# Performance work log

Hardware: AMD Instinct MI355X
Metric: run time of the kernel (lower is better)

## Reference

```python
import jax, jax.numpy as jnp
import numpy as np

DIM = 128
N_VAR = 100000
N_CON = 100000
N_NODES = 200000
N_EDGES = 640000


def setup_inputs() -> dict:
    key = jax.random.key(0)
    ks = jax.random.split(key, 25)
    d = DIM
    u = lambda k, s: jax.random.uniform(k, s, jnp.float32, -0.1, 0.1)
    inp = {
        "var_node_features": jax.random.normal(ks[0], (N_VAR, 2), jnp.float32),
        "con_node_features": jax.random.normal(ks[1], (N_CON, 2), jnp.float32),
        "node_types": jax.random.randint(ks[2], (N_NODES,), 0, 2),
        "assoc_var": jnp.arange(N_VAR),
        "assoc_con": N_VAR + jnp.arange(N_CON),
        "edge_index": jax.random.randint(ks[3], (2, N_EDGES), 0, N_NODES),
        "edge_types": jax.random.randint(ks[4], (N_EDGES,), 0, 2),
        "edge_features": jax.random.normal(ks[5], (N_EDGES, 1), jnp.float32),
        "var_w1": u(ks[6], (2, d)), "var_b1": u(ks[7], (d,)),
        "var_w2": u(ks[8], (d, d)), "var_b2": u(ks[9], (d,)),
        "con_w1": u(ks[10], (2, d)), "con_b1": u(ks[11], (d,)),
        "con_w2": u(ks[12], (d, d)), "con_b2": u(ks[13], (d,)),
    }
    for i, k0 in zip((1, 2, 3), (14, 17, 20)):
        inp[f"basis{i}"] = u(ks[k0], (1, d, d))      # num_bases=1
        inp[f"att{i}"] = u(ks[k0 + 1], (2, 1))       # num_relations=2
        inp[f"root{i}"] = u(ks[k0 + 2], (d, d))
        inp[f"bias{i}"] = jnp.zeros((d,), jnp.float32)
    inp["fc1_w"] = u(ks[23], (4 * d, d))
    inp["fc1_b"] = jnp.zeros((d,), jnp.float32)
    inp["fc4_w"] = u(ks[24], (d, 1))
    inp["fc4_b"] = jnp.zeros((1,), jnp.float32)
    return inp


def rgcn(x, src, dst, etype, basis, att, root, bias):
    # basis: [1, d, d], att: [2, 1] -> per-relation weights [2, d, d]
    d = x.shape[-1]
    w = (att @ basis.reshape(basis.shape[0], -1)).reshape(2, d, d)
    xj = x[src]  # [E, d] gather
    # only 2 relations: two GEMMs + select (avoids [E,d,d] materialization)
    msg = jnp.where((etype == 0)[:, None], xj @ w[0], xj @ w[1])
    s = jax.ops.segment_sum(msg, dst, num_segments=N_NODES)
    cnt = jax.ops.segment_sum(jnp.ones((dst.shape[0],), x.dtype), dst, num_segments=N_NODES)
    agg = s / jnp.maximum(cnt, 1.0)[:, None]  # mean aggregation
    return agg + x @ root + bias


def reference(var_node_features, con_node_features, node_types, assoc_var, assoc_con,
              edge_index, edge_types, edge_features,
              var_w1, var_b1, var_w2, var_b2,
              con_w1, con_b1, con_w2, con_b2,
              basis1, att1, root1, bias1,
              basis2, att2, root2, bias2,
              basis3, att3, root3, bias3,
              fc1_w, fc1_b, fc4_w, fc4_b):
    n = jnp.maximum(var_node_features @ var_w1 + var_b1, 0.0) @ var_w2 + var_b2
    e = jnp.maximum(con_node_features @ con_w1 + con_b1, 0.0) @ con_w2 + con_b2
    x = jnp.zeros((node_types.shape[0], n.shape[-1]), n.dtype)
    x = x.at[assoc_var].set(n).at[assoc_con].set(e)
    src, dst = edge_index[0], edge_index[1]
    x1 = jax.nn.relu(rgcn(x, src, dst, edge_types, basis1, att1, root1, bias1))
    x2 = jax.nn.relu(rgcn(x1, src, dst, edge_types, basis2, att2, root2, bias2))
    x3 = jax.nn.relu(rgcn(x2, src, dst, edge_types, basis3, att3, root3, bias3))
    h = jnp.concatenate([x, x1, x2, x3], axis=-1)[assoc_var]  # [n_var, 4d]
    h = jax.nn.relu(h @ fc1_w + fc1_b)
    # dropout p=0.5 is identity in eval mode
    return (h @ fc4_w + fc4_b)[:, 0]
```

## Files before the change

kernel.cpp:

```cpp
#include <hip/hip_runtime.h>
#include <hip/hip_bf16.h>

#define D 128
#define NV 100000
#define NC 100000
#define NN 200000
#define NE 640000

typedef __attribute__((ext_vector_type(4))) float f32x4;
typedef __attribute__((ext_vector_type(8))) short bf16x8;

static __device__ __forceinline__ unsigned short f2b(float f) {
    __hip_bfloat16 h = __float2bfloat16(f);
    union { __hip_bfloat16 h; unsigned short u; } c; c.h = h; return c.u;
}
static __device__ __forceinline__ float b2f(unsigned short b) {
    union { unsigned int u; float f; } c; c.u = ((unsigned int)b) << 16; return c.f;
}

template<bool RELU>
static __device__ __forceinline__ void split8v(const float f[8], bf16x8& ah, bf16x8& al)
{
    union { unsigned short s[8]; bf16x8 v; } ph, pl;
    #pragma unroll
    for (int j = 0; j < 8; ++j) {
        float x = RELU ? fmaxf(f[j], 0.f) : f[j];
        ph.s[j] = f2b(x);
        pl.s[j] = f2b(x - b2f(ph.s[j]));
    }
    ah = ph.v; al = pl.v;
}

union H8 { _Float16 h[8]; uint4 u; };
union H4 { _Float16 h[4]; uint2 u; };

struct PrepArgs { const float* src[12]; };

__global__ __launch_bounds__(256, 1) void prep_kernel(PrepArgs a, unsigned short* wt)
{
    const float* W = a.src[blockIdx.y];
    unsigned short* hi = wt + (size_t)blockIdx.y * 32768;
    unsigned short* lo = hi + 16384;
    const int o = blockIdx.x * 1024 + threadIdx.x * 4;
    const int slice = o >> 10;
    const int n     = (o >> 3) & 127;
    const int j0    = o & 7;
    union { unsigned short s[4]; unsigned long long u; } ph, pl;
    #pragma unroll
    for (int i = 0; i < 4; ++i) {
        const int k = slice * 8 + j0 + i;
        const float w = W[k * 128 + n];
        ph.s[i] = f2b(w);
        pl.s[i] = f2b(w - b2f(ph.s[i]));
    }
    *(unsigned long long*)&hi[o] = ph.u;
    *(unsigned long long*)&lo[o] = pl.u;
}

static __device__ __forceinline__ const bf16x8* wfrag(const unsigned short* wt,
                                                      int ks, int lg, int n)
{
    return (const bf16x8*)(wt + (((ks * 4 + lg) * 128) + n) * 8);
}

static __device__ __forceinline__ char* haddr(char* base, int row, int byteoff)
{
    return base + row * 256 + (byteoff ^ ((row & 7) << 4));
}

template<bool RELU, bool HASAGG>
static __device__ __forceinline__ void wsplit8(uint4 xv, uint4 gv,
                                               char* hb, char* lb, int srow, int ob0)
{
    H8 a0; a0.u = xv;
    float f[8];
    #pragma unroll
    for (int j = 0; j < 8; ++j) f[j] = (float)a0.h[j];
    if (HASAGG) {
        H8 g0; g0.u = gv;
        #pragma unroll
        for (int j = 0; j < 8; ++j) f[j] += (float)g0.h[j];
    }
    bf16x8 h0, l0;
    split8v<RELU>(f, h0, l0);
    *(bf16x8*)(hb + srow * 256 + ob0) = h0;
    *(bf16x8*)(lb + srow * 256 + ob0) = l0;
}

template<int AMODE, bool RELU_A, bool ADD_C>
__global__ __launch_bounds__(256, 4) void gemm6(
    const void* A, const _Float16* __restrict__ agg,
    const float* __restrict__ w1, const float* __restrict__ b1, int M,
    const unsigned short* __restrict__ wt, const float* __restrict__ bias,
    _Float16* Cout)
{
    __shared__ unsigned short Hs[2][2][32 * 128];
    const int tid  = threadIdx.x;
    const int lane = tid & 63, wv = tid >> 6;
    const int li   = lane & 15, lg = lane >> 4;
    const int colbase = wv * 32;

    bf16x8 bh[4][2], bl[4][2];
    #pragma unroll
    for (int ks = 0; ks < 4; ++ks)
        #pragma unroll
        for (int nf = 0; nf < 2; ++nf) {
            const int n = colbase + nf * 16 + li;
            bh[ks][nf] = *wfrag(wt,         ks, lg, n);
            bl[ks][nf] = *wfrag(wt + 16384, ks, lg, n);
        }

    const int ntiles = (M + 31) / 32;
    const int G = gridDim.x;
    const int t0 = blockIdx.x;
    if (t0 >= ntiles) return;

    const int srow = tid >> 3;
    const int skf  = (tid & 7) * 16;
    const int sw   = (srow & 7) << 4;
    const int ob0  = (skf * 2) ^ sw;
    const int ob1  = (skf * 2 + 16) ^ sw;

    #define LOADT(TT, XV0, XV1, GV0, GV1, FV)                                    \
    {                                                                            \
        int grow = (TT) * 32 + srow; if (grow >= M) grow = M - 1;                \
        if (AMODE == 2) {                                                        \
            FV = *(const float2*)((const float*)A + (size_t)grow * 2);           \
        } else {                                                                 \
            const uint4* ap = (const uint4*)((const _Float16*)A + (size_t)grow * D + skf); \
            XV0 = ap[0]; XV1 = ap[1];                                            \
            if (AMODE == 1) {                                                    \
                const uint4* gp = (const uint4*)(agg + (size_t)grow * D + skf);  \
                GV0 = gp[0]; GV1 = gp[1];                                        \
            }                                                                    \
        }                                                                        \
    }
    #define WRITET(BUF, XV0, XV1, GV0, GV1, FV)                                  \
    {                                                                            \
        char* hb_ = (char*)&Hs[BUF][0][0];                                       \
        char* lb_ = (char*)&Hs[BUF][1][0];                                       \
        if (AMODE == 2) {                                                        \
            float f[16];                                                         \
            const float f0 = FV.x, f1 = FV.y;                                    \
            _Pragma("unroll")                                                    \
            for (int q = 0; q < 4; ++q) {                                        \
                const float4 wa = *(const float4*)(w1 + skf + q * 4);            \
                const float4 wb = *(const float4*)(w1 + 128 + skf + q * 4);      \
                const float4 bb = *(const float4*)(b1 + skf + q * 4);            \
                f[q*4+0] = fmaxf(fmaf(f0, wa.x, fmaf(f1, wb.x, bb.x)), 0.f);     \
                f[q*4+1] = fmaxf(fmaf(f0, wa.y, fmaf(f1, wb.y, bb.y)), 0.f);     \
                f[q*4+2] = fmaxf(fmaf(f0, wa.z, fmaf(f1, wb.z, bb.z)), 0.f);     \
                f[q*4+3] = fmaxf(fmaf(f0, wa.w, fmaf(f1, wb.w, bb.w)), 0.f);     \
            }                                                                    \
            bf16x8 h0, l0, h1, l1;                                               \
            split8v<RELU_A>(&f[0], h0, l0);                                     \
            split8v<RELU_A>(&f[8], h1, l1);                                     \
            char* hbr = hb_ + srow * 256; char* lbr = lb_ + srow * 256;          \
            *(bf16x8*)(hbr + ob0) = h0; *(bf16x8*)(hbr + ob1) = h1;              \
            *(bf16x8*)(lbr + ob0) = l0; *(bf16x8*)(lbr + ob1) = l1;              \
        } else {                                                                 \
            wsplit8<RELU_A, AMODE == 1>(XV0, GV0, hb_, lb_, srow, ob0);          \
            wsplit8<RELU_A, AMODE == 1>(XV1, GV1, hb_, lb_, srow, ob1);          \
        }                                                                        \
    }

    {
        uint4 xv0 = {0,0,0,0}, xv1 = {0,0,0,0}, gv0 = {0,0,0,0}, gv1 = {0,0,0,0};
        float2 fv = {0, 0};
        LOADT(t0, xv0, xv1, gv0, gv1, fv);
        WRITET(0, xv0, xv1, gv0, gv1, fv);
    }
    __syncthreads();

    int cur = 0;
    for (int t = t0; t < ntiles; t += G) {
        const int tn = t + G;
        const bool pf = tn < ntiles;
        uint4 xv0 = {0,0,0,0}, xv1 = {0,0,0,0}, gv0 = {0,0,0,0}, gv1 = {0,0,0,0};
        float2 fv = {0, 0};
        if (pf) LOADT(tn, xv0, xv1, gv0, gv1, fv);

        char* hb = (char*)&Hs[cur][0][0];
        char* lb = (char*)&Hs[cur][1][0];
        f32x4 acc[2][2];
        #pragma unroll
        for (int ms = 0; ms < 2; ++ms)
            #pragma unroll
            for (int nf = 0; nf < 2; ++nf) acc[ms][nf] = (f32x4){0.f, 0.f, 0.f, 0.f};
        #pragma unroll
        for (int ks = 0; ks < 4; ++ks) {
            const int kb = ks * 64 + lg * 16;
            bf16x8 ah[2], al[2];
            #pragma unroll
            for (int ms = 0; ms < 2; ++ms) {
                const int row = ms * 16 + li;
                ah[ms] = *(const bf16x8*)haddr(hb, row, kb);
                al[ms] = *(const bf16x8*)haddr(lb, row, kb);
            }
            #pragma unroll
            for (int nf = 0; nf < 2; ++nf)
                #pragma unroll
                for (int ms = 0; ms < 2; ++ms) {
                    acc[ms][nf] = __builtin_amdgcn_mfma_f32_16x16x32_bf16(bh[ks][nf], ah[ms], acc[ms][nf], 0, 0, 0);
                    acc[ms][nf] = __builtin_amdgcn_mfma_f32_16x16x32_bf16(bh[ks][nf], al[ms], acc[ms][nf], 0, 0, 0);
                    acc[ms][nf] = __builtin_amdgcn_mfma_f32_16x16x32_bf16(bl[ks][nf], ah[ms], acc[ms][nf], 0, 0, 0);
                }
        }

        #pragma unroll
        for (int ms = 0; ms < 2; ++ms) {
            const int grow = t * 32 + ms * 16 + li;
            if (grow < M) {
                _Float16* crow = Cout + (size_t)grow * D;
                #pragma unroll
                for (int nf = 0; nf < 2; ++nf) {
                    const int c0 = colbase + nf * 16 + lg * 4;
                    float v[4];
                    #pragma unroll
                    for (int r = 0; r < 4; ++r) v[r] = acc[ms][nf][r];
                    if (bias) {
                        const float4 b = *(const float4*)(bias + c0);
                        v[0] += b.x; v[1] += b.y; v[2] += b.z; v[3] += b.w;
                    }
                    if (ADD_C) {
                        H4 rd; rd.u = *(const uint2*)(crow + c0);
                        #pragma unroll
                        for (int r = 0; r < 4; ++r) v[r] += (float)rd.h[r];
                    }
                    H4 pk;
                    #pragma unroll
                    for (int r = 0; r < 4; ++r) pk.h[r] = (_Float16)v[r];
                    *(uint2*)(crow + c0) = pk.u;
                }
            }
        }

        if (pf) WRITET(cur ^ 1, xv0, xv1, gv0, gv1, fv);
        __syncthreads();
        cur ^= 1;
    }
    #undef LOADT
    #undef WRITET
}

template<bool RELU_A, bool HASAGG, bool UADD>
__global__ __launch_bounds__(768, 3) void layer6(
    _Float16* x, const _Float16* __restrict__ agg, int M, int Mroot,
    const unsigned short* __restrict__ wtb, const unsigned short* __restrict__ wtr,
    const unsigned short* __restrict__ wtu, const float* __restrict__ bias,
    unsigned short* __restrict__ y, _Float16* __restrict__ u, int Mu)
{
    __shared__ unsigned short Hs[2][2][32 * 128];
    const int tid  = threadIdx.x;
    const int lane = tid & 63, wv = tid >> 6;
    const int li   = lane & 15, lg = lane >> 4;
    const int wgrp = wv >> 2;
    const int colbase = (wv & 3) * 32;
    const unsigned short* wsel = (wgrp == 0) ? wtb : (wgrp == 1) ? wtr : wtu;

    bf16x8 bh[4][2], bl[4][2];
    #pragma unroll
    for (int ks = 0; ks < 4; ++ks)
        #pragma unroll
        for (int nf = 0; nf < 2; ++nf) {
            const int n = colbase + nf * 16 + li;
            bh[ks][nf] = *wfrag(wsel,         ks, lg, n);
            bl[ks][nf] = *wfrag(wsel + 16384, ks, lg, n);
        }
    float4 bv[2] = {{0,0,0,0},{0,0,0,0}};
    if (wgrp == 1) {
        bv[0] = *(const float4*)(bias + colbase + 0  + lg * 4);
        bv[1] = *(const float4*)(bias + colbase + 16 + lg * 4);
    }

    const int ntiles = (M + 31) / 32;
    const int G = gridDim.x;
    const int t0 = blockIdx.x;
    if (t0 >= ntiles) return;

    const bool stager = tid < 512;
    const int srow = (tid & 511) >> 4;
    const int skf  = (tid & 15) * 8;
    const int sw   = (srow & 7) << 4;
    const int ob0  = (skf * 2) ^ sw;

    if (stager) {
        int grow = t0 * 32 + srow; if (grow >= M) grow = M - 1;
        uint4 xv = *(const uint4*)(x + (size_t)grow * D + skf);
        uint4 gv = {0,0,0,0};
        if (HASAGG) gv = *(const uint4*)(agg + (size_t)grow * D + skf);
        wsplit8<RELU_A, HASAGG>(xv, gv, (char*)&Hs[0][0][0], (char*)&Hs[0][1][0], srow, ob0);
    }
    __syncthreads();

    int cur = 0;
    for (int t = t0; t < ntiles; t += G) {
        const int tn = t + G;
        const bool pf = stager && (tn < ntiles);
        uint4 xv = {0,0,0,0}, gv = {0,0,0,0};
        if (pf) {
            int grow = tn * 32 + srow; if (grow >= M) grow = M - 1;
            xv = *(const uint4*)(x + (size_t)grow * D + skf);
            if (HASAGG) gv = *(const uint4*)(agg + (size_t)grow * D + skf);
        }

        char* hb = (char*)&Hs[cur][0][0];
        char* lb = (char*)&Hs[cur][1][0];
        f32x4 acc[2][2];
        #pragma unroll
        for (int ms = 0; ms < 2; ++ms)
            #pragma unroll
            for (int nf = 0; nf < 2; ++nf) acc[ms][nf] = (f32x4){0.f, 0.f, 0.f, 0.f};
        #pragma unroll
        for (int ks = 0; ks < 4; ++ks) {
            const int kb = ks * 64 + lg * 16;
            bf16x8 ah[2], al[2];
            #pragma unroll
            for (int ms = 0; ms < 2; ++ms) {
                const int row = ms * 16 + li;
                ah[ms] = *(const bf16x8*)haddr(hb, row, kb);
                al[ms] = *(const bf16x8*)haddr(lb, row, kb);
            }
            #pragma unroll
            for (int nf = 0; nf < 2; ++nf)
                #pragma unroll
                for (int ms = 0; ms < 2; ++ms) {
                    acc[ms][nf] = __builtin_amdgcn_mfma_f32_16x16x32_bf16(bh[ks][nf], ah[ms], acc[ms][nf], 0, 0, 0);
                    acc[ms][nf] = __builtin_amdgcn_mfma_f32_16x16x32_bf16(bh[ks][nf], al[ms], acc[ms][nf], 0, 0, 0);
                    acc[ms][nf] = __builtin_amdgcn_mfma_f32_16x16x32_bf16(bl[ks][nf], ah[ms], acc[ms][nf], 0, 0, 0);
                }
        }

        #pragma unroll
        for (int ms = 0; ms < 2; ++ms) {
            const int grow = t * 32 + ms * 16 + li;
            if (wgrp == 0) {
                if (grow < M) {
                    unsigned short* yrow = y + (size_t)grow * D;
                    #pragma unroll
                    for (int nf = 0; nf < 2; ++nf) {
                        const int c0 = colbase + nf * 16 + lg * 4;
                        union { unsigned short s[4]; uint2 v; } pk;
                        #pragma unroll
                        for (int r = 0; r < 4; ++r) pk.s[r] = f2b(acc[ms][nf][r]);
                        *(uint2*)(yrow + c0) = pk.v;
                    }
                }
            } else if (wgrp == 1) {
                if (grow < Mroot) {
                    _Float16* xrow = x + (size_t)grow * D;
                    #pragma unroll
                    for (int nf = 0; nf < 2; ++nf) {
                        const int c0 = colbase + nf * 16 + lg * 4;
                        const float bb[4] = {bv[nf].x, bv[nf].y, bv[nf].z, bv[nf].w};
                        H4 pk;
                        #pragma unroll
                        for (int r = 0; r < 4; ++r) pk.h[r] = (_Float16)(acc[ms][nf][r] + bb[r]);
                        *(uint2*)(xrow + c0) = pk.u;
                    }
                }
            } else {
                if (grow < Mu) {
                    _Float16* urow = u + (size_t)grow * D;
                    #pragma unroll
                    for (int nf = 0; nf < 2; ++nf) {
                        const int c0 = colbase + nf * 16 + lg * 4;
                        float v[4];
                        #pragma unroll
                        for (int r = 0; r < 4; ++r) v[r] = acc[ms][nf][r];
                        if (UADD) {
                            H4 rd; rd.u = *(const uint2*)(urow + c0);
                            #pragma unroll
                            for (int r = 0; r < 4; ++r) v[r] += (float)rd.h[r];
                        }
                        H4 pk;
                        #pragma unroll
                        for (int r = 0; r < 4; ++r) pk.h[r] = (_Float16)v[r];
                        *(uint2*)(urow + c0) = pk.u;
                    }
                }
            }
        }

        if (pf)
            wsplit8<RELU_A, HASAGG>(xv, gv, (char*)&Hs[cur ^ 1][0][0],
                                    (char*)&Hs[cur ^ 1][1][0], srow, ob0);
        __syncthreads();
        cur ^= 1;
    }
}

__global__ void hist_kernel(const int* __restrict__ dst, int* __restrict__ deg, int ne)
{
    int g = blockIdx.x * blockDim.x + threadIdx.x;
    if (g < ne) atomicAdd(&deg[dst[g]], 1);
}

__global__ __launch_bounds__(256, 1) void scan_blk(int* __restrict__ buf,
                                                   int* __restrict__ sums, int n)
{
    __shared__ int part[256];
    const int tid  = threadIdx.x;
    const int base = blockIdx.x * 1024 + tid * 4;
    int v0 = (base + 0 < n) ? buf[base + 0] : 0;
    int v1 = (base + 1 < n) ? buf[base + 1] : 0;
    int v2 = (base + 2 < n) ? buf[base + 2] : 0;
    int v3 = (base + 3 < n) ? buf[base + 3] : 0;
    const int t0 = v0, t1 = t0 + v1, t2 = t1 + v2, t3 = t2 + v3;
    part[tid] = t3;
    __syncthreads();
    #pragma unroll
    for (int off = 1; off < 256; off <<= 1) {
        int x = part[tid];
        if (tid >= off) x += part[tid - off];
        __syncthreads();
        part[tid] = x;
        __syncthreads();
    }
    if (tid == 255) sums[blockIdx.x] = part[255];
    const int excl = tid ? part[tid - 1] : 0;
    if (base + 0 < n) buf[base + 0] = excl;
    if (base + 1 < n) buf[base + 1] = excl + t0;
    if (base + 2 < n) buf[base + 2] = excl + t1;
    if (base + 3 < n) buf[base + 3] = excl + t2;
}

__global__ __launch_bounds__(256, 1) void scan_top(int* __restrict__ sums, int nb)
{
    __shared__ int part[256];
    const int tid = threadIdx.x;
    part[tid] = (tid < nb) ? sums[tid] : 0;
    __syncthreads();
    #pragma unroll
    for (int off = 1; off < 256; off <<= 1) {
        int x = part[tid];
        if (tid >= off) x += part[tid - off];
        __syncthreads();
        part[tid] = x;
        __syncthreads();
    }
    if (tid < nb) sums[tid] = tid ? part[tid - 1] : 0;
}

__global__ void scan_add(int* __restrict__ buf, const int* __restrict__ sums, int n)
{
    int i = blockIdx.x * blockDim.x + threadIdx.x;
    if (i < n) buf[i] += sums[i >> 10];
}

__global__ void fill_kernel(const int* __restrict__ src, const int* __restrict__ dst,
                            const int* __restrict__ etype,
                            int* __restrict__ cursor, int* __restrict__ edges, int ne)
{
    int e = blockIdx.x * blockDim.x + threadIdx.x;
    if (e < ne) {
        const int pos = atomicAdd(&cursor[dst[e]], 1);
        edges[pos] = (src[e] << 1) | (etype[e] & 1);
    }
}

__global__ __launch_bounds__(256, 2) void gather_agg(
    const int* __restrict__ cursor, const int* __restrict__ edges,
    const float* __restrict__ att, const unsigned short* __restrict__ y,
    _Float16* __restrict__ agg, int nn)
{
    const int gid  = blockIdx.x * 256 + threadIdx.x;
    const int node = gid >> 4;
    const int l    = gid & 15;
    if (node >= nn) return;
    const int end   = cursor[node];
    const int start = node ? cursor[node - 1] : 0;
    const float a0 = att[0], a1 = att[1];
    float s0[8] = {0,0,0,0,0,0,0,0}, s1[8] = {0,0,0,0,0,0,0,0};
    int j = start;
    for (; j + 2 <= end; j += 2) {
        const int p0 = edges[j], p1 = edges[j + 1];
        const float w0 = (p0 & 1) ? a1 : a0;
        const float w1 = (p1 & 1) ? a1 : a0;
        const uint4 va = ((const uint4*)(y + ((size_t)(p0 >> 1)) * D))[l];
        const uint4 vb = ((const uint4*)(y + ((size_t)(p1 >> 1)) * D))[l];
        const unsigned int wa[4] = {va.x, va.y, va.z, va.w};
        const unsigned int wb[4] = {vb.x, vb.y, vb.z, vb.w};
        #pragma unroll
        for (int q = 0; q < 4; ++q) {
            s0[q * 2 + 0] = fmaf(w0, b2f((unsigned short)(wa[q] & 0xFFFF)), s0[q * 2 + 0]);
            s0[q * 2 + 1] = fmaf(w0, b2f((unsigned short)(wa[q] >> 16)),    s0[q * 2 + 1]);
            s1[q * 2 + 0] = fmaf(w1, b2f((unsigned short)(wb[q] & 0xFFFF)), s1[q * 2 + 0]);
            s1[q * 2 + 1] = fmaf(w1, b2f((unsigned short)(wb[q] >> 16)),    s1[q * 2 + 1]);
        }
    }
    if (j < end) {
        const int p0 = edges[j];
        const float w0 = (p0 & 1) ? a1 : a0;
        const uint4 va = ((const uint4*)(y + ((size_t)(p0 >> 1)) * D))[l];
        const unsigned int wa[4] = {va.x, va.y, va.z, va.w};
        #pragma unroll
        for (int q = 0; q < 4; ++q) {
            s0[q * 2 + 0] = fmaf(w0, b2f((unsigned short)(wa[q] & 0xFFFF)), s0[q * 2 + 0]);
            s0[q * 2 + 1] = fmaf(w0, b2f((unsigned short)(wa[q] >> 16)),    s0[q * 2 + 1]);
        }
    }
    const float inv = 1.0f / fmaxf((float)(end - start), 1.0f);
    H8 o;
    #pragma unroll
    for (int q = 0; q < 8; ++q) o.h[q] = (_Float16)((s0[q] + s1[q]) * inv);
    *(uint4*)(agg + (size_t)node * D + l * 8) = o.u;
}

__global__ void final_kernel(
    const _Float16* __restrict__ u, const float* __restrict__ fc1_b,
    const float* __restrict__ fc4_w, const float* __restrict__ fc4_b,
    float* __restrict__ out, int n)
{
    int gid = blockIdx.x * blockDim.x + threadIdx.x;
    int row = gid >> 5, lane = gid & 31;
    if (row >= n) return;
    H4 uv; uv.u = ((const uint2*)(u + (size_t)row * D))[lane];
    float4 b = ((const float4*)fc1_b)[lane];
    float4 w = ((const float4*)fc4_w)[lane];
    float s = fmaxf((float)uv.h[0] + b.x, 0.f) * w.x
            + fmaxf((float)uv.h[1] + b.y, 0.f) * w.y
            + fmaxf((float)uv.h[2] + b.z, 0.f) * w.z
            + fmaxf((float)uv.h[3] + b.w, 0.f) * w.w;
    #pragma unroll
    for (int off = 1; off < 32; off <<= 1) s += __shfl_xor(s, off);
    if (lane == 0) out[row] = s + fc4_b[0];
}

extern "C" void kernel_launch(void* const* d_in, const int* in_sizes, int n_in,
                              void* d_out, int out_size, void* d_ws, size_t ws_size,
                              hipStream_t stream)
{
    const float* varf      = (const float*)d_in[0];
    const float* conf      = (const float*)d_in[1];
    const int*   edge_src  = (const int*)d_in[5];
    const int*   edge_dst  = edge_src + NE;
    const int*   etype     = (const int*)d_in[6];
    const float* var_w1 = (const float*)d_in[8];
    const float* var_b1 = (const float*)d_in[9];
    const float* var_w2 = (const float*)d_in[10];
    const float* var_b2 = (const float*)d_in[11];
    const float* con_w1 = (const float*)d_in[12];
    const float* con_b1 = (const float*)d_in[13];
    const float* con_w2 = (const float*)d_in[14];
    const float* con_b2 = (const float*)d_in[15];
    const float* basisL[3] = {(const float*)d_in[16], (const float*)d_in[20], (const float*)d_in[24]};
    const float* attL[3]   = {(const float*)d_in[17], (const float*)d_in[21], (const float*)d_in[25]};
    const float* rootL[3]  = {(const float*)d_in[18], (const float*)d_in[22], (const float*)d_in[26]};
    const float* biasL[3]  = {(const float*)d_in[19], (const float*)d_in[23], (const float*)d_in[27]};
    const float* fc1_w = (const float*)d_in[28];
    const float* fc1_b = (const float*)d_in[29];
    const float* fc4_w = (const float*)d_in[30];
    const float* fc4_b = (const float*)d_in[31];

    const size_t XB  = (size_t)NN * D * 2;
    const size_t YB  = (size_t)NN * D * 2;
    const size_t AB  = (size_t)NN * D * 2;
    const size_t UB  = (size_t)NV * D * 2;
    const size_t CUR = (size_t)NN * 4;
    const size_t EDG = (size_t)NE * 4;
    const size_t SUM = 4096;
    const size_t WT  = (size_t)12 * 32768 * 2;
    const size_t need = XB + YB + AB + UB + CUR + EDG + SUM + WT;
    if (ws_size < need) {
        hipMemsetAsync(d_out, 0, (size_t)out_size * sizeof(float), stream);
        return;
    }
    char* p = (char*)d_ws;
    _Float16*       x      = (_Float16*)p;       p += XB;
    unsigned short* y      = (unsigned short*)p; p += YB;
    _Float16*       agg    = (_Float16*)p;       p += AB;
    _Float16*       u      = (_Float16*)p;       p += UB;
    int*            cursor = (int*)p;            p += CUR;
    int*            edges  = (int*)p;            p += EDG;
    int*            sums   = (int*)p;            p += SUM;
    unsigned short* wt     = (unsigned short*)p;

    PrepArgs pa;
    pa.src[0] = basisL[0]; pa.src[1] = basisL[1]; pa.src[2] = basisL[2];
    pa.src[3] = rootL[0];  pa.src[4] = rootL[1];  pa.src[5] = rootL[2];
    pa.src[6] = fc1_w;                 pa.src[7] = fc1_w + 128 * 128;
    pa.src[8] = fc1_w + 2 * 128 * 128; pa.src[9] = fc1_w + 3 * 128 * 128;
    pa.src[10] = var_w2;               pa.src[11] = con_w2;
    prep_kernel<<<dim3(16, 12), 256, 0, stream>>>(pa, wt);

    hipMemsetAsync(cursor, 0, CUR, stream);
    hist_kernel<<<(NE + 255) / 256, 256, 0, stream>>>(edge_dst, cursor, NE);
    const int nblk = (NN + 1023) / 1024;
    scan_blk<<<nblk, 256, 0, stream>>>(cursor, sums, NN);
    scan_top<<<1, 256, 0, stream>>>(sums, nblk);
    scan_add<<<(NN + 255) / 256, 256, 0, stream>>>(cursor, sums, NN);
    fill_kernel<<<(NE + 255) / 256, 256, 0, stream>>>(edge_src, edge_dst, etype,
                                                      cursor, edges, NE);

    const int GM = 1024;
    const int GL = 256;

    gemm6<2, false, false><<<GM, 256, 0, stream>>>(
        varf, nullptr, var_w1, var_b1, NV, wt + (size_t)10 * 32768, var_b2, x);
    gemm6<2, false, false><<<GM, 256, 0, stream>>>(
        conf, nullptr, con_w1, con_b1, NC, wt + (size_t)11 * 32768, con_b2,
        x + (size_t)NV * D);

    for (int l = 0; l < 3; ++l) {
        const unsigned short* wb_ = wt + (size_t)l * 32768;
        const unsigned short* wr_ = wt + (size_t)(3 + l) * 32768;
        const unsigned short* wu_ = wt + (size_t)(6 + l) * 32768;
        const int mroot = (l == 2) ? NV : NN;
        const int gn    = (l == 2) ? NV : NN;
        if (l == 0)
            layer6<false, false, false><<<GL, 768, 0, stream>>>(
                x, nullptr, NN, mroot, wb_, wr_, wu_, biasL[0], y, u, NV);
        else
            layer6<true, true, true><<<GL, 768, 0, stream>>>(
                x, agg, NN, mroot, wb_, wr_, wu_, biasL[l], y, u, NV);
        gather_agg<<<(gn * 16 + 255) / 256, 256, 0, stream>>>(
            cursor, edges, attL[l], y, agg, gn);
    }

    gemm6<1, true, true><<<GM, 256, 0, stream>>>(
        x, agg, nullptr, nullptr, NV, wt + (size_t)9 * 32768, nullptr, u);

    final_kernel<<<(NV * 32 + 255) / 256, 256, 0, stream>>>(
        u, fc1_b, fc4_w, fc4_b, (float*)d_out, NV);
}
```

Before: 411.9 us.

## Double layer GEMM row tile to 64 and skip idle wave-group work

```diff
diff --git a/kernel.cpp b/kernel.cpp
--- a/kernel.cpp
+++ b/kernel.cpp
@@ -244,13 +244,13 @@
 }
 
 template<bool RELU_A, bool HASAGG, bool UADD>
-__global__ __launch_bounds__(768, 3) void layer6(
+__global__ __launch_bounds__(768, 6) void layer7(
     _Float16* x, const _Float16* __restrict__ agg, int M, int Mroot,
     const unsigned short* __restrict__ wtb, const unsigned short* __restrict__ wtr,
     const unsigned short* __restrict__ wtu, const float* __restrict__ bias,
     unsigned short* __restrict__ y, _Float16* __restrict__ u, int Mu)
 {
-    __shared__ unsigned short Hs[2][2][32 * 128];
+    __shared__ unsigned short Hs[2][2][64 * 128];
     const int tid  = threadIdx.x;
     const int lane = tid & 63, wv = tid >> 6;
     const int li   = lane & 15, lg = lane >> 4;
@@ -273,23 +273,29 @@
         bv[1] = *(const float4*)(bias + colbase + 16 + lg * 4);
     }
 
-    const int ntiles = (M + 31) / 32;
+    const int ntiles = (M + 63) / 64;
     const int G = gridDim.x;
     const int t0 = blockIdx.x;
     if (t0 >= ntiles) return;
 
     const bool stager = tid < 512;
-    const int srow = (tid & 511) >> 4;
-    const int skf  = (tid & 15) * 8;
+    const int srow = (tid & 511) >> 3;
+    const int skf  = (tid & 7) * 16;
     const int sw   = (srow & 7) << 4;
     const int ob0  = (skf * 2) ^ sw;
+    const int ob1  = (skf * 2 + 16) ^ sw;
 
     if (stager) {
-        int grow = t0 * 32 + srow; if (grow >= M) grow = M - 1;
-        uint4 xv = *(const uint4*)(x + (size_t)grow * D + skf);
-        uint4 gv = {0,0,0,0};
-        if (HASAGG) gv = *(const uint4*)(agg + (size_t)grow * D + skf);
-        wsplit8<RELU_A, HASAGG>(xv, gv, (char*)&Hs[0][0][0], (char*)&Hs[0][1][0], srow, ob0);
+        int grow = t0 * 64 + srow; if (grow >= M) grow = M - 1;
+        const uint4* ap = (const uint4*)(x + (size_t)grow * D + skf);
+        uint4 xv0 = ap[0], xv1 = ap[1];
+        uint4 gv0 = {0,0,0,0}, gv1 = {0,0,0,0};
+        if (HASAGG) {
+            const uint4* gp = (const uint4*)(agg + (size_t)grow * D + skf);
+            gv0 = gp[0]; gv1 = gp[1];
+        }
+        wsplit8<RELU_A, HASAGG>(xv0, gv0, (char*)&Hs[0][0][0], (char*)&Hs[0][1][0], srow, ob0);
+        wsplit8<RELU_A, HASAGG>(xv1, gv1, (char*)&Hs[0][0][0], (char*)&Hs[0][1][0], srow, ob1);
     }
     __syncthreads();
 
@@ -297,94 +303,105 @@
     for (int t = t0; t < ntiles; t += G) {
         const int tn = t + G;
         const bool pf = stager && (tn < ntiles);
-        uint4 xv = {0,0,0,0}, gv = {0,0,0,0};
+        uint4 xv0 = {0,0,0,0}, xv1 = {0,0,0,0}, gv0 = {0,0,0,0}, gv1 = {0,0,0,0};
         if (pf) {
-            int grow = tn * 32 + srow; if (grow >= M) grow = M - 1;
-            xv = *(const uint4*)(x + (size_t)grow * D + skf);
-            if (HASAGG) gv = *(const uint4*)(agg + (size_t)grow * D + skf);
-        }
-
-        char* hb = (char*)&Hs[cur][0][0];
-        char* lb = (char*)&Hs[cur][1][0];
-        f32x4 acc[2][2];
-        #pragma unroll
-        for (int ms = 0; ms < 2; ++ms)
+            int grow = tn * 64 + srow; if (grow >= M) grow = M - 1;
+            const uint4* ap = (const uint4*)(x + (size_t)grow * D + skf);
+            xv0 = ap[0]; xv1 = ap[1];
+            if (HASAGG) {
+                const uint4* gp = (const uint4*)(agg + (size_t)grow * D + skf);
+                gv0 = gp[0]; gv1 = gp[1];
+            }
+        }
+
+        const bool dowork = (wgrp == 0) ||
+                            (wgrp == 1 ? (t * 64 < Mroot) : (t * 64 < Mu));
+        if (dowork) {
+            char* hb = (char*)&Hs[cur][0][0];
+            char* lb = (char*)&Hs[cur][1][0];
+            f32x4 acc[4][2];
             #pragma unroll
-            for (int nf = 0; nf < 2; ++nf) acc[ms][nf] = (f32x4){0.f, 0.f, 0.f, 0.f};
-        #pragma unroll
-        for (int ks = 0; ks < 4; ++ks) {
-            const int kb = ks * 64 + lg * 16;
-            bf16x8 ah[2], al[2];
+            for (int ms = 0; ms < 4; ++ms)
+                #pragma unroll
+                for (int nf = 0; nf < 2; ++nf) acc[ms][nf] = (f32x4){0.f, 0.f, 0.f, 0.f};
             #pragma unroll
-            for (int ms = 0; ms < 2; ++ms) {
-                const int row = ms * 16 + li;
-                ah[ms] = *(const bf16x8*)haddr(hb, row, kb);
-                al[ms] = *(const bf16x8*)haddr(lb, row, kb);
+            for (int ks = 0; ks < 4; ++ks) {
+                const int kb = ks * 64 + lg * 16;
+                bf16x8 ah[4], al[4];
+                #pragma unroll
+                for (int ms = 0; ms < 4; ++ms) {
+                    const int row = ms * 16 + li;
+                    ah[ms] = *(const bf16x8*)haddr(hb, row, kb);
+                    al[ms] = *(const bf16x8*)haddr(lb, row, kb);
+                }
+                #pragma unroll
+                for (int nf = 0; nf < 2; ++nf)
+                    #pragma unroll
+                    for (int ms = 0; ms < 4; ++ms) {
+                        acc[ms][nf] = __builtin_amdgcn_mfma_f32_16x16x32_bf16(bh[ks][nf], ah[ms], acc[ms][nf], 0, 0, 0);
+                        acc[ms][nf] = __builtin_amdgcn_mfma_f32_16x16x32_bf16(bh[ks][nf], al[ms], acc[ms][nf], 0, 0, 0);
+                        acc[ms][nf] = __builtin_amdgcn_mfma_f32_16x16x32_bf16(bl[ks][nf], ah[ms], acc[ms][nf], 0, 0, 0);
+                    }
             }
+
             #pragma unroll
-            for (int nf = 0; nf < 2; ++nf)
-                #pragma unroll
-                for (int ms = 0; ms < 2; ++ms) {
-                    acc[ms][nf] = __builtin_amdgcn_mfma_f32_16x16x32_bf16(bh[ks][nf], ah[ms], acc[ms][nf], 0, 0, 0);
-                    acc[ms][nf] = __builtin_amdgcn_mfma_f32_16x16x32_bf16(bh[ks][nf], al[ms], acc[ms][nf], 0, 0, 0);
-                    acc[ms][nf] = __builtin_amdgcn_mfma_f32_16x16x32_bf16(bl[ks][nf], ah[ms], acc[ms][nf], 0, 0, 0);
-                }
-        }
-
-        #pragma unroll
-        for (int ms = 0; ms < 2; ++ms) {
-            const int grow = t * 32 + ms * 16 + li;
-            if (wgrp == 0) {
-                if (grow < M) {
-                    unsigned short* yrow = y + (size_t)grow * D;
-                    #pragma unroll
-                    for (int nf = 0; nf < 2; ++nf) {
-                        const int c0 = colbase + nf * 16 + lg * 4;
-                        union { unsigned short s[4]; uint2 v; } pk;
+            for (int ms = 0; ms < 4; ++ms) {
+                const int gr = t * 64 + ms * 16 + li;
+                if (wgrp == 0) {
+                    if (gr < M) {
+                        unsigned short* yrow = y + (size_t)gr * D;
                         #pragma unroll
-                        for (int r = 0; r < 4; ++r) pk.s[r] = f2b(acc[ms][nf][r]);
-                        *(uint2*)(yrow + c0) = pk.v;
+                        for (int nf = 0; nf < 2; ++nf) {
+                            const int c0 = colbase + nf * 16 + lg * 4;
+                            union { unsigned short s[4]; uint2 v; } pk;
+                            #pragma unroll
+                            for (int r = 0; r < 4; ++r) pk.s[r] = f2b(acc[ms][nf][r]);
+                            *(uint2*)(yrow + c0) = pk.v;
+                        }
                     }
-                }
-            } else if (wgrp == 1) {
-                if (grow < Mroot) {
-                    _Float16* xrow = x + (size_t)grow * D;
-                    #pragma unroll
-                    for (int nf = 0; nf < 2; ++nf) {
-                        const int c0 = colbase + nf * 16 + lg * 4;
-                        const float bb[4] = {bv[nf].x, bv[nf].y, bv[nf].z, bv[nf].w};
-                        H4 pk;
+                } else if (wgrp == 1) {
+                    if (gr < Mroot) {
+                        _Float16* xrow = x + (size_t)gr * D;
                         #pragma unroll
-                        for (int r = 0; r < 4; ++r) pk.h[r] = (_Float16)(acc[ms][nf][r] + bb[r]);
-                        *(uint2*)(xrow + c0) = pk.u;
+                        for (int nf = 0; nf < 2; ++nf) {
+                            const int c0 = colbase + nf * 16 + lg * 4;
+                            const float bb[4] = {bv[nf].x, bv[nf].y, bv[nf].z, bv[nf].w};
+                            H4 pk;
+                            #pragma unroll
+                            for (int r = 0; r < 4; ++r) pk.h[r] = (_Float16)(acc[ms][nf][r] + bb[r]);
+                            *(uint2*)(xrow + c0) = pk.u;
+                        }
                     }
-                }
-            } else {
-                if (grow < Mu) {
-                    _Float16* urow = u + (size_t)grow * D;
-                    #pragma unroll
-                    for (int nf = 0; nf < 2; ++nf) {
-                        const int c0 = colbase + nf * 16 + lg * 4;
-                        float v[4];
+                } else {
+                    if (gr < Mu) {
+                        _Float16* urow = u + (size_t)gr * D;
                         #pragma unroll
-                        for (int r = 0; r < 4; ++r) v[r] = acc[ms][nf][r];
-                        if (UADD) {
-                            H4 rd; rd.u = *(const uint2*)(urow + c0);
+                        for (int nf = 0; nf < 2; ++nf) {
+                            const int c0 = colbase + nf * 16 + lg * 4;
+                            float v[4];
                             #pragma unroll
-                            for (int r = 0; r < 4; ++r) v[r] += (float)rd.h[r];
+                            for (int r = 0; r < 4; ++r) v[r] = acc[ms][nf][r];
+                            if (UADD) {
+                                H4 rd; rd.u = *(const uint2*)(urow + c0);
+                                #pragma unroll
+                                for (int r = 0; r < 4; ++r) v[r] += (float)rd.h[r];
+                            }
+                            H4 pk;
+                            #pragma unroll
+                            for (int r = 0; r < 4; ++r) pk.h[r] = (_Float16)v[r];
+                            *(uint2*)(urow + c0) = pk.u;
                         }
-                        H4 pk;
-                        #pragma unroll
-                        for (int r = 0; r < 4; ++r) pk.h[r] = (_Float16)v[r];
-                        *(uint2*)(urow + c0) = pk.u;
                     }
                 }
             }
         }
 
-        if (pf)
-            wsplit8<RELU_A, HASAGG>(xv, gv, (char*)&Hs[cur ^ 1][0][0],
+        if (pf) {
+            wsplit8<RELU_A, HASAGG>(xv0, gv0, (char*)&Hs[cur ^ 1][0][0],
                                     (char*)&Hs[cur ^ 1][1][0], srow, ob0);
+            wsplit8<RELU_A, HASAGG>(xv1, gv1, (char*)&Hs[cur ^ 1][0][0],
+                                    (char*)&Hs[cur ^ 1][1][0], srow, ob1);
+        }
         __syncthreads();
         cur ^= 1;
     }
@@ -594,7 +611,7 @@
                                                       cursor, edges, NE);
 
     const int GM = 1024;
-    const int GL = 256;
+    const int GL = 512;
 
     gemm6<2, false, false><<<GM, 256, 0, stream>>>(
         varf, nullptr, var_w1, var_b1, NV, wt + (size_t)10 * 32768, var_b2, x);
@@ -609,10 +626,10 @@
         const int mroot = (l == 2) ? NV : NN;
         const int gn    = (l == 2) ? NV : NN;
         if (l == 0)
-            layer6<false, false, false><<<GL, 768, 0, stream>>>(
+            layer7<false, false, false><<<GL, 768, 0, stream>>>(
                 x, nullptr, NN, mroot, wb_, wr_, wu_, biasL[0], y, u, NV);
         else
-            layer6<true, true, true><<<GL, 768, 0, stream>>>(
+            layer7<true, true, true><<<GL, 768, 0, stream>>>(
                 x, agg, NN, mroot, wb_, wr_, wu_, biasL[l], y, u, NV);
         gather_agg<<<(gn * 16 + 255) / 256, 256, 0, stream>>>(
             cursor, edges, attL[l], y, agg, gn);
```

Measured after the change: 784.3 us. 1.9x slower.
